# Kernel optimization log

Hardware: AMD Instinct MI355X
Metric: run time of the kernel (lower is better)

## Reference

```python
import jax, jax.numpy as jnp
import numpy as np

B, A, D, H = 32, 64, 128, 512
F = A * D  # 8192

def setup_inputs() -> dict:
    key = jax.random.key(0)
    ks = jax.random.split(key, 20)
    s = 0.02
    return {
        "swarm_states": jax.random.normal(ks[0], (B, A, D), jnp.float32),
        "swarm_goals": jax.random.normal(ks[1], (B, A, D), jnp.float32),
        # quantum layer stand-in: Linear(F->F) + tanh
        "Wq": jax.random.normal(ks[2], (F, F), jnp.float32) * s,
        "bq": jnp.zeros((F,), jnp.float32),
        # interaction_net: Linear(2D->H) ReLU Linear(H->H) ReLU Linear(H->D)
        "Wi1": jax.random.normal(ks[3], (2 * D, H), jnp.float32) * s,
        "bi1": jnp.zeros((H,), jnp.float32),
        "Wi2": jax.random.normal(ks[4], (H, H), jnp.float32) * s,
        "bi2": jnp.zeros((H,), jnp.float32),
        "Wi3": jax.random.normal(ks[5], (H, D), jnp.float32) * s,
        "bi3": jnp.zeros((D,), jnp.float32),
        # coordination_net: Linear(F->H) ReLU Linear(H->H) ReLU Linear(H->F)
        "Wc1": jax.random.normal(ks[6], (F, H), jnp.float32) * s,
        "bc1": jnp.zeros((H,), jnp.float32),
        "Wc2": jax.random.normal(ks[7], (H, H), jnp.float32) * s,
        "bc2": jnp.zeros((H,), jnp.float32),
        "Wc3": jax.random.normal(ks[8], (H, F), jnp.float32) * s,
        "bc3": jnp.zeros((F,), jnp.float32),
    }

def reference(swarm_states, swarm_goals, Wq, bq, Wi1, bi1, Wi2, bi2, Wi3, bi3,
              Wc1, bc1, Wc2, bc2, Wc3, bc3):
    b, a, d = swarm_states.shape
    states_flat = swarm_states.reshape(b, a * d)
    # quantum feature extraction (stand-in for QuantumNeuralLayer)
    quantum_features = jnp.tanh(states_flat @ Wq + bq)  # (B, A*D)

    # vectorized pairwise interaction MLP over all ordered (i, j) pairs
    xi = jnp.broadcast_to(swarm_states[:, :, None, :], (b, a, a, d))
    xj = jnp.broadcast_to(swarm_states[:, None, :, :], (b, a, a, d))
    pair = jnp.concatenate([xi, xj], axis=-1)            # (B, A, A, 2D)
    h = jax.nn.relu(pair @ Wi1 + bi1)
    h = jax.nn.relu(h @ Wi2 + bi2)
    inter = h @ Wi3 + bi3                                # (B, A, A, D)
    offdiag = (1.0 - jnp.eye(a, dtype=inter.dtype))[None, :, :, None]
    # per-agent aggregation over the other agents (mean over j != i)
    interactions = (inter * offdiag).sum(axis=2) / (a - 1)  # (B, A, D)

    c = jax.nn.relu(quantum_features @ Wc1 + bc1)
    c = jax.nn.relu(c @ Wc2 + bc2)
    coordination = (c @ Wc3 + bc3).reshape(b, a, d)      # (B, A, D)

    coordinated_states = swarm_states + 0.1 * interactions + 0.1 * coordination
    return coordinated_states, quantum_features, interactions, coordination
```

## Files before the change

### kernel.cpp

```cpp
#include <hip/hip_runtime.h>

typedef __attribute__((ext_vector_type(8))) short bf16x8;
typedef __attribute__((ext_vector_type(16))) float f32x16;
typedef _Float16 f16;
typedef __attribute__((ext_vector_type(8))) _Float16 f16x8;

static __device__ __forceinline__ unsigned short f2bf(float x) {
  unsigned int u = __float_as_uint(x);
  return (unsigned short)((u + 0x7FFFu + ((u >> 16) & 1u)) >> 16);
}
static __device__ __forceinline__ unsigned int pk2bf(float lo, float hi) {
  return ((unsigned int)f2bf(hi) << 16) | f2bf(lo);
}

static __device__ __forceinline__ f16x8 relu8(f16x8 x) {
  f16x8 z = {0, 0, 0, 0, 0, 0, 0, 0};
  return __builtin_elementwise_max(x, z);
}

__global__ __launch_bounds__(256) void tobf_kernel(const float* __restrict__ src,
                                                   unsigned short* __restrict__ dst) {
  const int idx = blockIdx.x * 256 + threadIdx.x;
  float4 v = ((const float4*)src)[idx];
  ushort4 o;
  o.x = f2bf(v.x); o.y = f2bf(v.y); o.z = f2bf(v.z); o.w = f2bf(v.w);
  ((ushort4*)dst)[idx] = o;
}

__global__ __launch_bounds__(256) void w2h_kernel(const float* __restrict__ Wi2,
                                                  f16* __restrict__ W2h) {
  __shared__ float tile[32][33];
  const int t = threadIdx.x;
  const int bk = blockIdx.x, bn = blockIdx.y;
  const int r = t >> 5, c = t & 31;
#pragma unroll
  for (int p = 0; p < 4; p++) {
    int rr = p * 8 + r;
    tile[rr][c] = Wi2[(bk * 32 + rr) * 512 + bn * 32 + c];
  }
  __syncthreads();
#pragma unroll
  for (int p = 0; p < 4; p++) {
    int rr = p * 8 + r;
    W2h[(bn * 32 + rr) * 512 + bk * 32 + c] = (f16)tile[c][rr];
  }
}

__global__ __launch_bounds__(256) void uvh_kernel(const float* __restrict__ S,
                                                  const float* __restrict__ Wi1,
                                                  const float* __restrict__ bi1,
                                                  f16* __restrict__ Uh, f16* __restrict__ Vh) {
  __shared__ float st[128][12];
  const int t = threadIdx.x;
  const int row0 = blockIdx.x * 8;
  for (int idx = t; idx < 1024; idx += 256) {
    int r = idx >> 7, k = idx & 127;
    st[k][r] = S[(row0 + r) * 128 + k];
  }
  __syncthreads();
  float au0[8], au1[8], av0[8], av1[8];
#pragma unroll
  for (int r = 0; r < 8; r++) { au0[r] = 0.f; au1[r] = 0.f; av0[r] = 0.f; av1[r] = 0.f; }
#pragma unroll 4
  for (int k = 0; k < 128; k++) {
    float wt0 = Wi1[k * 512 + t];
    float wt1 = Wi1[k * 512 + 256 + t];
    float wb0 = Wi1[(k + 128) * 512 + t];
    float wb1 = Wi1[(k + 128) * 512 + 256 + t];
    float4 sA = *(const float4*)&st[k][0];
    float4 sB = *(const float4*)&st[k][4];
    float s8[8] = {sA.x, sA.y, sA.z, sA.w, sB.x, sB.y, sB.z, sB.w};
#pragma unroll
    for (int r = 0; r < 8; r++) {
      au0[r] += s8[r] * wt0;
      au1[r] += s8[r] * wt1;
      av0[r] += s8[r] * wb0;
      av1[r] += s8[r] * wb1;
    }
  }
  const float b0 = bi1[t], b1 = bi1[256 + t];
#pragma unroll
  for (int r = 0; r < 8; r++) {
    Uh[(row0 + r) * 512 + t]       = (f16)(au0[r] + b0);
    Uh[(row0 + r) * 512 + 256 + t] = (f16)(au1[r] + b1);
    Vh[(row0 + r) * 512 + t]       = (f16)av0[r];
    Vh[(row0 + r) * 512 + 256 + t] = (f16)av1[r];
  }
}

__global__ __launch_bounds__(256, 4) void gemmw(const unsigned short* __restrict__ Abf,
                                                const float* __restrict__ W,
                                                float* __restrict__ P,
                                                int K, int N, int L, int l4sh) {
  __shared__ __align__(16) unsigned short As[32 * 512];
  const int t = threadIdx.x;
  const int k0 = blockIdx.y * L;
  const int L4 = L >> 2;
  const int swzm = 2 * L - 1;
  for (int idx = t; idx < (L << 3); idx += 256) {
    int row = idx >> l4sh, k4 = idx & (L4 - 1);
    ushort4 a4 = *(const ushort4*)&Abf[(size_t)row * K + k0 + k4 * 4];
    int off = (row * 2 * L + k4 * 8) ^ (((row & 7) << 4) & swzm);
    *(ushort4*)((char*)As + off) = a4;
  }
  __syncthreads();
  const int lane = t & 63, w = t >> 6;
  const int lrow = lane & 31, lh = lane >> 5;
  const int col = blockIdx.x * 128 + w * 32 + lrow;
  f32x16 acc0, acc1;
#pragma unroll
  for (int r = 0; r < 16; r++) { acc0[r] = 0.f; acc1[r] = 0.f; }
  const float* Wp = W + (size_t)(k0 + lh * 8) * N + col;
  const int aswz = ((lrow & 7) << 4) & swzm;
  const int abase = lrow * 2 * L + lh * 16;
  const int nks = L >> 4;
  int ks = 0;
  for (; ks + 1 < nks; ks += 2) {
    float wv0[8], wv1[8];
#pragma unroll
    for (int jj = 0; jj < 8; jj++) wv0[jj] = Wp[(size_t)(ks * 16 + jj) * N];
#pragma unroll
    for (int jj = 0; jj < 8; jj++) wv1[jj] = Wp[(size_t)(ks * 16 + 16 + jj) * N];
    uint4 b0, b1;
    b0.x = pk2bf(wv0[0], wv0[1]); b0.y = pk2bf(wv0[2], wv0[3]);
    b0.z = pk2bf(wv0[4], wv0[5]); b0.w = pk2bf(wv0[6], wv0[7]);
    b1.x = pk2bf(wv1[0], wv1[1]); b1.y = pk2bf(wv1[2], wv1[3]);
    b1.z = pk2bf(wv1[4], wv1[5]); b1.w = pk2bf(wv1[6], wv1[7]);
    bf16x8 af0 = *(const bf16x8*)((const char*)As + ((abase + ks * 32) ^ aswz));
    bf16x8 af1 = *(const bf16x8*)((const char*)As + ((abase + ks * 32 + 32) ^ aswz));
    acc0 = __builtin_amdgcn_mfma_f32_32x32x16_bf16(af0, *(const bf16x8*)&b0, acc0, 0, 0, 0);
    acc1 = __builtin_amdgcn_mfma_f32_32x32x16_bf16(af1, *(const bf16x8*)&b1, acc1, 0, 0, 0);
  }
  if (ks < nks) {
    float wv0[8];
#pragma unroll
    for (int jj = 0; jj < 8; jj++) wv0[jj] = Wp[(size_t)(ks * 16 + jj) * N];
    uint4 b0;
    b0.x = pk2bf(wv0[0], wv0[1]); b0.y = pk2bf(wv0[2], wv0[3]);
    b0.z = pk2bf(wv0[4], wv0[5]); b0.w = pk2bf(wv0[6], wv0[7]);
    bf16x8 af0 = *(const bf16x8*)((const char*)As + ((abase + ks * 32) ^ aswz));
    acc0 = __builtin_amdgcn_mfma_f32_32x32x16_bf16(af0, *(const bf16x8*)&b0, acc0, 0, 0, 0);
  }
  float* Pr = P + (size_t)blockIdx.y * 32 * N + col;
#pragma unroll
  for (int r = 0; r < 16; r++) {
    int row = (r & 3) + 8 * (r >> 2) + 4 * lh;
    Pr[(size_t)row * N] = acc0[r] + acc1[r];
  }
}

__global__ __launch_bounds__(256) void reduce_kernel(const float* __restrict__ P,
                                                     const float* __restrict__ bias,
                                                     float* __restrict__ dst,
                                                     unsigned short* __restrict__ dstbf,
                                                     int lnN, int KS, int act, int wbf) {
  const int idx = blockIdx.x * 256 + threadIdx.x;
  const int N = 1 << lnN;
  const int m = idx >> lnN, n = idx & (N - 1);
  float s = 0.f;
#pragma unroll 8
  for (int p = 0; p < KS; p++) s += P[((size_t)(p * 32 + m) << lnN) + n];
  s += bias[n];
  if (act == 1) s = fmaxf(s, 0.f);
  else if (act == 2) s = tanhf(s);
  dst[idx] = s;
  if (wbf) dstbf[idx] = f2bf(s);
}

__global__ __launch_bounds__(512, 2) void inter5_kernel(const f16* __restrict__ Uh,
                                                        const f16* __restrict__ Vh,
                                                        const f16* __restrict__ W2h,
                                                        const float* __restrict__ bi2,
                                                        float* __restrict__ Hsum) {
  __shared__ __align__(16) f16 Bt[128 * 512];
  const int t = threadIdx.x;
  const int nq = blockIdx.x;

#pragma unroll
  for (int i = 0; i < 16; i++) {
    int idx = i * 512 + t;
    int n = idx >> 6, ch = idx & 63;
    f16x8 w8 = *(const f16x8*)&W2h[(size_t)(nq * 128 + n) * 512 + ch * 8];
    int off = (n * 1024 + ch * 16) ^ ((n & 15) << 4);
    *(f16x8*)((char*)Bt + off) = w8;
  }
  __syncthreads();

  const int w = t >> 6, lane = t & 63;
  const int ii = w & 1, tg = w >> 1;
  const int lrow = lane & 31, lh = lane >> 5;
  const char* Btc = (const char*)Bt;

  int bofs[4], bswz[4];
#pragma unroll
  for (int nf = 0; nf < 4; nf++) {
    int nr = nf * 32 + lrow;
    bofs[nf] = nr * 1024 + lh * 16;
    bswz[nf] = (nr & 15) << 4;
  }

  for (int s = 0; s < 4; s++) {
    const int tid = blockIdx.y * 16 + tg * 4 + s;
    const int b = tid >> 5, it = tid & 31;
    const f16* Vb0 = Vh + (size_t)(b * 64 + lrow) * 512 + lh * 8;
    const f16* Vb1 = Vb0 + (size_t)32 * 512;
    const f16* Ub = Uh + (size_t)(b * 64 + it * 2 + ii) * 512 + lh * 8;

    f32x16 acc[2][4];
#pragma unroll
    for (int mf = 0; mf < 2; mf++)
#pragma unroll
      for (int nf = 0; nf < 4; nf++)
#pragma unroll
        for (int r = 0; r < 16; r++) acc[mf][nf][r] = 0.f;

    f16x8 v0 = *(const f16x8*)(Vb0);
    f16x8 v1 = *(const f16x8*)(Vb1);
    f16x8 u0 = *(const f16x8*)(Ub);
    f16x8 bf[4];
#pragma unroll
    for (int nf = 0; nf < 4; nf++) bf[nf] = *(const f16x8*)(Btc + (bofs[nf] ^ bswz[nf]));

#pragma unroll 2
    for (int kc = 0; kc < 512; kc += 16) {
      const int kn = (kc + 16) & 511;
      f16x8 v0n = *(const f16x8*)(Vb0 + kn);
      f16x8 v1n = *(const f16x8*)(Vb1 + kn);
      f16x8 u0n = *(const f16x8*)(Ub + kn);
      f16x8 bfn[4];
#pragma unroll
      for (int nf = 0; nf < 4; nf++)
        bfn[nf] = *(const f16x8*)(Btc + ((bofs[nf] + kn * 2) ^ bswz[nf]));
      f16x8 a0 = relu8(v0 + u0);
      f16x8 a1 = relu8(v1 + u0);
#pragma unroll
      for (int nf = 0; nf < 4; nf++) {
        acc[0][nf] = __builtin_amdgcn_mfma_f32_32x32x16_f16(a0, bf[nf], acc[0][nf], 0, 0, 0);
        acc[1][nf] = __builtin_amdgcn_mfma_f32_32x32x16_f16(a1, bf[nf], acc[1][nf], 0, 0, 0);
      }
      v0 = v0n; v1 = v1n; u0 = u0n;
#pragma unroll
      for (int nf = 0; nf < 4; nf++) bf[nf] = bfn[nf];
    }

    const int iglob = it * 2 + ii;
    const int mf_d = iglob >> 5;
    const int rd = iglob & 31;
    const int lh_d = (rd >> 2) & 1;
    const int r_d = (rd & 3) + 4 * (rd >> 3);
#pragma unroll
    for (int nf = 0; nf < 4; nf++) {
      const int col = nq * 128 + nf * 32 + lrow;
      const float b2 = bi2[col];
      float ssum = 0.f;
#pragma unroll
      for (int mf = 0; mf < 2; mf++)
#pragma unroll
        for (int r = 0; r < 16; r++) {
          float x = fmaxf(acc[mf][nf][r] + b2, 0.f);
          if (mf == mf_d && r == r_d && lh == lh_d) x = 0.f;
          ssum += x;
        }
      ssum += __shfl_xor(ssum, 32);
      if (lh == 0) Hsum[(size_t)(b * 64 + iglob) * 512 + col] = ssum;
    }
  }
}

__global__ __launch_bounds__(256) void k3_kernel(const float* __restrict__ Hsum,
                                                 const float* __restrict__ Wi3,
                                                 const float* __restrict__ bi3,
                                                 float* __restrict__ inter) {
  __shared__ float st[512][20];
  const int t = threadIdx.x;
  const int row0 = blockIdx.x * 16;
  for (int idx = t; idx < 8192; idx += 256) {
    int r = idx >> 9, k = idx & 511;
    st[k][r] = Hsum[(row0 + r) * 512 + k] * (1.0f / 63.0f);
  }
  __syncthreads();
  const int c = t & 63;
  const int rg = t >> 6;
  float a0[4] = {0.f, 0.f, 0.f, 0.f}, a1[4] = {0.f, 0.f, 0.f, 0.f};
#pragma unroll 4
  for (int k = 0; k < 512; k++) {
    float w0 = Wi3[k * 128 + c];
    float w1 = Wi3[k * 128 + 64 + c];
    float4 h = *(const float4*)&st[k][rg * 4];
    a0[0] += h.x * w0; a0[1] += h.y * w0; a0[2] += h.z * w0; a0[3] += h.w * w0;
    a1[0] += h.x * w1; a1[1] += h.y * w1; a1[2] += h.z * w1; a1[3] += h.w * w1;
  }
  float b0 = bi3[c], b1 = bi3[64 + c];
#pragma unroll
  for (int r = 0; r < 4; r++) {
    inter[(row0 + rg * 4 + r) * 128 + c]      = a0[r] + b0;
    inter[(row0 + rg * 4 + r) * 128 + 64 + c] = a1[r] + b1;
  }
}

__global__ __launch_bounds__(256) void combine_kernel(const float* __restrict__ S,
                                                      const float* __restrict__ inter,
                                                      const float* __restrict__ coord,
                                                      float* __restrict__ out0) {
  const int i = blockIdx.x * 256 + threadIdx.x;
  float4 s = ((const float4*)S)[i];
  float4 a = ((const float4*)inter)[i];
  float4 c = ((const float4*)coord)[i];
  float4 o;
  o.x = s.x + 0.1f * (a.x + c.x);
  o.y = s.y + 0.1f * (a.y + c.y);
  o.z = s.z + 0.1f * (a.z + c.z);
  o.w = s.w + 0.1f * (a.w + c.w);
  ((float4*)out0)[i] = o;
}

extern "C" void kernel_launch(void* const* d_in, const int* in_sizes, int n_in,
                              void* d_out, int out_size, void* d_ws, size_t ws_size,
                              hipStream_t stream) {
  const float* states = (const float*)d_in[0];
  const float* Wq  = (const float*)d_in[2];
  const float* bq  = (const float*)d_in[3];
  const float* Wi1 = (const float*)d_in[4];
  const float* bi1 = (const float*)d_in[5];
  const float* Wi2 = (const float*)d_in[6];
  const float* bi2 = (const float*)d_in[7];
  const float* Wi3 = (const float*)d_in[8];
  const float* bi3 = (const float*)d_in[9];
  const float* Wc1 = (const float*)d_in[10];
  const float* bc1 = (const float*)d_in[11];
  const float* Wc2 = (const float*)d_in[12];
  const float* bc2 = (const float*)d_in[13];
  const float* Wc3 = (const float*)d_in[14];
  const float* bc3 = (const float*)d_in[15];

  float* out   = (float*)d_out;
  float* out0  = out;
  float* qf    = out + 262144;
  float* inter = out + 524288;
  float* coord = out + 786432;

  char* ws = (char*)d_ws;
  float*          P    = (float*)(ws);
  f16*            Uh   = (f16*)(ws + ((size_t)16 << 20));
  f16*            Vh   = (f16*)(ws + ((size_t)19 << 20));
  f16*            W2h  = (f16*)(ws + ((size_t)22 << 20));
  float*          Hsum = (float*)(ws + ((size_t)23 << 20));
  unsigned short* Sbf  = (unsigned short*)(ws + ((size_t)27 << 20));
  unsigned short* qfbf = (unsigned short*)(ws + ((size_t)28 << 20));
  float*          c1   = (float*)(ws + ((size_t)29 << 20));
  float*          c2   = (float*)(ws + ((size_t)29 << 20) + (1 << 16));
  unsigned short* c1bf = (unsigned short*)(ws + ((size_t)29 << 20) + (2 << 16));
  unsigned short* c2bf = (unsigned short*)(ws + ((size_t)29 << 20) + (3 << 16));

  tobf_kernel<<<256, 256, 0, stream>>>(states, Sbf);
  w2h_kernel<<<dim3(16, 16), 256, 0, stream>>>(Wi2, W2h);
  uvh_kernel<<<256, 256, 0, stream>>>(states, Wi1, bi1, Uh, Vh);

  gemmw<<<dim3(64, 16), 256, 0, stream>>>(Sbf, Wq, P, 8192, 8192, 512, 7);
  reduce_kernel<<<1024, 256, 0, stream>>>(P, bq, qf, qfbf, 13, 16, 2, 1);

  inter5_kernel<<<dim3(4, 64), 512, 0, stream>>>(Uh, Vh, W2h, bi2, Hsum);
  k3_kernel<<<128, 256, 0, stream>>>(Hsum, Wi3, bi3, inter);

  gemmw<<<dim3(4, 64), 256, 0, stream>>>(qfbf, Wc1, P, 8192, 512, 128, 5);
  reduce_kernel<<<64, 256, 0, stream>>>(P, bc1, c1, c1bf, 9, 64, 1, 1);
  gemmw<<<dim3(4, 32), 256, 0, stream>>>(c1bf, Wc2, P, 512, 512, 16, 2);
  reduce_kernel<<<64, 256, 0, stream>>>(P, bc2, c2, c2bf, 9, 32, 1, 1);
  gemmw<<<dim3(64, 8), 256, 0, stream>>>(c2bf, Wc3, P, 512, 8192, 64, 4);
  reduce_kernel<<<1024, 256, 0, stream>>>(P, bc3, coord, qfbf, 13, 8, 0, 0);

  combine_kernel<<<256, 256, 0, stream>>>(states, inter, coord, out0);
}
```

Baseline: 240.6 us.

## Stage V tiles in shared memory for pairwise MLP and shrink k3 tiles

The pairwise interaction kernel now loads the V operand cooperatively into a swizzled 64x128 LDS chunk per K-block and reuses it across all waves. This replaces each wave's redundant global loads of V. Every block serves a single batch element, and the old register double-buffering of V and B loads is dropped. The k3 projection kernel handles 8 rows per block instead of 16, doubling the grid for more parallelism, at the cost of extra syncs per chunk and more LDS use.

```diff
diff --git a/kernel.cpp b/kernel.cpp
--- a/kernel.cpp
+++ b/kernel.cpp
@@ -167,12 +167,13 @@
   if (wbf) dstbf[idx] = f2bf(s);
 }
 
-__global__ __launch_bounds__(512, 2) void inter5_kernel(const f16* __restrict__ Uh,
+__global__ __launch_bounds__(512, 2) void inter6_kernel(const f16* __restrict__ Uh,
                                                         const f16* __restrict__ Vh,
                                                         const f16* __restrict__ W2h,
                                                         const float* __restrict__ bi2,
                                                         float* __restrict__ Hsum) {
   __shared__ __align__(16) f16 Bt[128 * 512];
+  __shared__ __align__(16) f16 Vc[64 * 128];
   const int t = threadIdx.x;
   const int nq = blockIdx.x;
 
@@ -184,12 +185,13 @@
     int off = (n * 1024 + ch * 16) ^ ((n & 15) << 4);
     *(f16x8*)((char*)Bt + off) = w8;
   }
-  __syncthreads();
 
   const int w = t >> 6, lane = t & 63;
   const int ii = w & 1, tg = w >> 1;
   const int lrow = lane & 31, lh = lane >> 5;
   const char* Btc = (const char*)Bt;
+  const char* Vcc = (const char*)Vc;
+  char* Vcw = (char*)Vc;
 
   int bofs[4], bswz[4];
 #pragma unroll
@@ -198,12 +200,16 @@
     bofs[nf] = nr * 1024 + lh * 16;
     bswz[nf] = (nr & 15) << 4;
   }
+  const int vofs0 = lrow * 256;
+  const int vswz0 = (lrow & 15) << 4;
+  const int vofs1 = (lrow + 32) * 256;
+  const int vswz1 = vswz0;
+
+  const int b = blockIdx.y >> 1;
 
   for (int s = 0; s < 4; s++) {
     const int tid = blockIdx.y * 16 + tg * 4 + s;
-    const int b = tid >> 5, it = tid & 31;
-    const f16* Vb0 = Vh + (size_t)(b * 64 + lrow) * 512 + lh * 8;
-    const f16* Vb1 = Vb0 + (size_t)32 * 512;
+    const int it = tid & 31;
     const f16* Ub = Uh + (size_t)(b * 64 + it * 2 + ii) * 512 + lh * 8;
 
     f32x16 acc[2][4];
@@ -214,33 +220,34 @@
 #pragma unroll
         for (int r = 0; r < 16; r++) acc[mf][nf][r] = 0.f;
 
-    f16x8 v0 = *(const f16x8*)(Vb0);
-    f16x8 v1 = *(const f16x8*)(Vb1);
-    f16x8 u0 = *(const f16x8*)(Ub);
-    f16x8 bf[4];
-#pragma unroll
-    for (int nf = 0; nf < 4; nf++) bf[nf] = *(const f16x8*)(Btc + (bofs[nf] ^ bswz[nf]));
-
-#pragma unroll 2
-    for (int kc = 0; kc < 512; kc += 16) {
-      const int kn = (kc + 16) & 511;
-      f16x8 v0n = *(const f16x8*)(Vb0 + kn);
-      f16x8 v1n = *(const f16x8*)(Vb1 + kn);
-      f16x8 u0n = *(const f16x8*)(Ub + kn);
-      f16x8 bfn[4];
-#pragma unroll
-      for (int nf = 0; nf < 4; nf++)
-        bfn[nf] = *(const f16x8*)(Btc + ((bofs[nf] + kn * 2) ^ bswz[nf]));
-      f16x8 a0 = relu8(v0 + u0);
-      f16x8 a1 = relu8(v1 + u0);
-#pragma unroll
-      for (int nf = 0; nf < 4; nf++) {
-        acc[0][nf] = __builtin_amdgcn_mfma_f32_32x32x16_f16(a0, bf[nf], acc[0][nf], 0, 0, 0);
-        acc[1][nf] = __builtin_amdgcn_mfma_f32_32x32x16_f16(a1, bf[nf], acc[1][nf], 0, 0, 0);
+    for (int ch = 0; ch < 4; ch++) {
+      const int kc = ch * 128;
+      __syncthreads();
+#pragma unroll
+      for (int i = 0; i < 2; i++) {
+        int idx = i * 512 + t;
+        int row = idx >> 4, c8 = idx & 15;
+        f16x8 w8 = *(const f16x8*)&Vh[(size_t)(b * 64 + row) * 512 + kc + c8 * 8];
+        *(f16x8*)(Vcw + ((row * 256 + c8 * 16) ^ ((row & 15) << 4))) = w8;
       }
-      v0 = v0n; v1 = v1n; u0 = u0n;
-#pragma unroll
-      for (int nf = 0; nf < 4; nf++) bf[nf] = bfn[nf];
+      __syncthreads();
+#pragma unroll
+      for (int k16 = 0; k16 < 8; k16++) {
+        const int kb2 = k16 * 32 + lh * 16;
+        f16x8 v0 = *(const f16x8*)(Vcc + ((vofs0 + kb2) ^ vswz0));
+        f16x8 v1 = *(const f16x8*)(Vcc + ((vofs1 + kb2) ^ vswz1));
+        f16x8 u0 = *(const f16x8*)(Ub + kc + k16 * 16);
+        f16x8 a0 = relu8(v0 + u0);
+        f16x8 a1 = relu8(v1 + u0);
+        const int kbyte = (kc + k16 * 16) * 2 + lh * 16 - lh * 16;
+        (void)kbyte;
+#pragma unroll
+        for (int nf = 0; nf < 4; nf++) {
+          f16x8 bfr = *(const f16x8*)(Btc + ((bofs[nf] + (kc + k16 * 16) * 2) ^ bswz[nf]));
+          acc[0][nf] = __builtin_amdgcn_mfma_f32_32x32x16_f16(a0, bfr, acc[0][nf], 0, 0, 0);
+          acc[1][nf] = __builtin_amdgcn_mfma_f32_32x32x16_f16(a1, bfr, acc[1][nf], 0, 0, 0);
+        }
+      }
     }
 
     const int iglob = it * 2 + ii;
@@ -271,30 +278,30 @@
                                                  const float* __restrict__ Wi3,
                                                  const float* __restrict__ bi3,
                                                  float* __restrict__ inter) {
-  __shared__ float st[512][20];
-  const int t = threadIdx.x;
-  const int row0 = blockIdx.x * 16;
-  for (int idx = t; idx < 8192; idx += 256) {
+  __shared__ float st[512][10];
+  const int t = threadIdx.x;
+  const int row0 = blockIdx.x * 8;
+  for (int idx = t; idx < 4096; idx += 256) {
     int r = idx >> 9, k = idx & 511;
     st[k][r] = Hsum[(row0 + r) * 512 + k] * (1.0f / 63.0f);
   }
   __syncthreads();
   const int c = t & 63;
   const int rg = t >> 6;
-  float a0[4] = {0.f, 0.f, 0.f, 0.f}, a1[4] = {0.f, 0.f, 0.f, 0.f};
+  float a0[2] = {0.f, 0.f}, a1[2] = {0.f, 0.f};
 #pragma unroll 4
   for (int k = 0; k < 512; k++) {
     float w0 = Wi3[k * 128 + c];
     float w1 = Wi3[k * 128 + 64 + c];
-    float4 h = *(const float4*)&st[k][rg * 4];
-    a0[0] += h.x * w0; a0[1] += h.y * w0; a0[2] += h.z * w0; a0[3] += h.w * w0;
-    a1[0] += h.x * w1; a1[1] += h.y * w1; a1[2] += h.z * w1; a1[3] += h.w * w1;
+    float2 h = *(const float2*)&st[k][rg * 2];
+    a0[0] += h.x * w0; a0[1] += h.y * w0;
+    a1[0] += h.x * w1; a1[1] += h.y * w1;
   }
   float b0 = bi3[c], b1 = bi3[64 + c];
 #pragma unroll
-  for (int r = 0; r < 4; r++) {
-    inter[(row0 + rg * 4 + r) * 128 + c]      = a0[r] + b0;
-    inter[(row0 + rg * 4 + r) * 128 + 64 + c] = a1[r] + b1;
+  for (int r = 0; r < 2; r++) {
+    inter[(row0 + rg * 2 + r) * 128 + c]      = a0[r] + b0;
+    inter[(row0 + rg * 2 + r) * 128 + 64 + c] = a1[r] + b1;
   }
 }
 
@@ -359,8 +366,8 @@
   gemmw<<<dim3(64, 16), 256, 0, stream>>>(Sbf, Wq, P, 8192, 8192, 512, 7);
   reduce_kernel<<<1024, 256, 0, stream>>>(P, bq, qf, qfbf, 13, 16, 2, 1);
 
-  inter5_kernel<<<dim3(4, 64), 512, 0, stream>>>(Uh, Vh, W2h, bi2, Hsum);
-  k3_kernel<<<128, 256, 0, stream>>>(Hsum, Wi3, bi3, inter);
+  inter6_kernel<<<dim3(4, 64), 512, 0, stream>>>(Uh, Vh, W2h, bi2, Hsum);
+  k3_kernel<<<256, 256, 0, stream>>>(Hsum, Wi3, bi3, inter);
 
   gemmw<<<dim3(4, 64), 256, 0, stream>>>(qfbf, Wc1, P, 8192, 512, 128, 5);
   reduce_kernel<<<64, 256, 0, stream>>>(P, bc1, c1, c1bf, 9, 64, 1, 1);
```

New measurement: 225.6 us. 6.2% less time.

## Reorder V to a k-blocked layout for coalesced MFMA loads, halve k3 rows per block

Applied to the files above, without the earlier changes.

The uvh kernel now writes V in a per-batch layout blocked by k-chunks of 8, so the 64 lanes of a wave load one contiguous 1 KB segment per k step in the pairwise MFMA kernel instead of striding across 1 KB rows. The interaction kernel's inner loop unroll is raised from 2 to 4. The k3 projection kernel processes 8 rows per block with 256 blocks instead of 16 rows with 128 blocks, for more parallelism. The scattered 2-byte stores in uvh may cost more, and the higher unroll raises register pressure.

```diff
diff --git a/kernel.cpp b/kernel.cpp
--- a/kernel.cpp
+++ b/kernel.cpp
@@ -49,7 +49,7 @@
 __global__ __launch_bounds__(256) void uvh_kernel(const float* __restrict__ S,
                                                   const float* __restrict__ Wi1,
                                                   const float* __restrict__ bi1,
-                                                  f16* __restrict__ Uh, f16* __restrict__ Vh) {
+                                                  f16* __restrict__ Uh, f16* __restrict__ Vg) {
   __shared__ float st[128][12];
   const int t = threadIdx.x;
   const int row0 = blockIdx.x * 8;
@@ -79,12 +79,15 @@
     }
   }
   const float b0 = bi1[t], b1 = bi1[256 + t];
+  const int kb = t >> 3, rem = t & 7;
 #pragma unroll
   for (int r = 0; r < 8; r++) {
-    Uh[(row0 + r) * 512 + t]       = (f16)(au0[r] + b0);
-    Uh[(row0 + r) * 512 + 256 + t] = (f16)(au1[r] + b1);
-    Vh[(row0 + r) * 512 + t]       = (f16)av0[r];
-    Vh[(row0 + r) * 512 + 256 + t] = (f16)av1[r];
+    const int row = row0 + r;
+    Uh[row * 512 + t]       = (f16)(au0[r] + b0);
+    Uh[row * 512 + 256 + t] = (f16)(au1[r] + b1);
+    const int j = row & 63, bb = row >> 6;
+    Vg[bb * 32768 + kb * 512 + j * 8 + rem]          = (f16)av0[r];
+    Vg[bb * 32768 + (kb + 32) * 512 + j * 8 + rem]   = (f16)av1[r];
   }
 }
 
@@ -167,8 +170,8 @@
   if (wbf) dstbf[idx] = f2bf(s);
 }
 
-__global__ __launch_bounds__(512, 2) void inter5_kernel(const f16* __restrict__ Uh,
-                                                        const f16* __restrict__ Vh,
+__global__ __launch_bounds__(512, 2) void inter7_kernel(const f16* __restrict__ Uh,
+                                                        const f16* __restrict__ Vg,
                                                         const f16* __restrict__ W2h,
                                                         const float* __restrict__ bi2,
                                                         float* __restrict__ Hsum) {
@@ -199,11 +202,12 @@
     bswz[nf] = (nr & 15) << 4;
   }
 
+  const int b = blockIdx.y >> 1;
+  const f16* Vbase = Vg + (size_t)b * 32768 + lh * 512 + lrow * 8;
+
   for (int s = 0; s < 4; s++) {
     const int tid = blockIdx.y * 16 + tg * 4 + s;
-    const int b = tid >> 5, it = tid & 31;
-    const f16* Vb0 = Vh + (size_t)(b * 64 + lrow) * 512 + lh * 8;
-    const f16* Vb1 = Vb0 + (size_t)32 * 512;
+    const int it = tid & 31;
     const f16* Ub = Uh + (size_t)(b * 64 + it * 2 + ii) * 512 + lh * 8;
 
     f32x16 acc[2][4];
@@ -214,18 +218,18 @@
 #pragma unroll
         for (int r = 0; r < 16; r++) acc[mf][nf][r] = 0.f;
 
-    f16x8 v0 = *(const f16x8*)(Vb0);
-    f16x8 v1 = *(const f16x8*)(Vb1);
+    f16x8 v0 = *(const f16x8*)(Vbase);
+    f16x8 v1 = *(const f16x8*)(Vbase + 256);
     f16x8 u0 = *(const f16x8*)(Ub);
     f16x8 bf[4];
 #pragma unroll
     for (int nf = 0; nf < 4; nf++) bf[nf] = *(const f16x8*)(Btc + (bofs[nf] ^ bswz[nf]));
 
-#pragma unroll 2
+#pragma unroll 4
     for (int kc = 0; kc < 512; kc += 16) {
       const int kn = (kc + 16) & 511;
-      f16x8 v0n = *(const f16x8*)(Vb0 + kn);
-      f16x8 v1n = *(const f16x8*)(Vb1 + kn);
+      f16x8 v0n = *(const f16x8*)(Vbase + kn * 64);
+      f16x8 v1n = *(const f16x8*)(Vbase + kn * 64 + 256);
       f16x8 u0n = *(const f16x8*)(Ub + kn);
       f16x8 bfn[4];
 #pragma unroll
@@ -271,30 +275,30 @@
                                                  const float* __restrict__ Wi3,
                                                  const float* __restrict__ bi3,
                                                  float* __restrict__ inter) {
-  __shared__ float st[512][20];
-  const int t = threadIdx.x;
-  const int row0 = blockIdx.x * 16;
-  for (int idx = t; idx < 8192; idx += 256) {
+  __shared__ float st[512][10];
+  const int t = threadIdx.x;
+  const int row0 = blockIdx.x * 8;
+  for (int idx = t; idx < 4096; idx += 256) {
     int r = idx >> 9, k = idx & 511;
     st[k][r] = Hsum[(row0 + r) * 512 + k] * (1.0f / 63.0f);
   }
   __syncthreads();
   const int c = t & 63;
   const int rg = t >> 6;
-  float a0[4] = {0.f, 0.f, 0.f, 0.f}, a1[4] = {0.f, 0.f, 0.f, 0.f};
+  float a0[2] = {0.f, 0.f}, a1[2] = {0.f, 0.f};
 #pragma unroll 4
   for (int k = 0; k < 512; k++) {
     float w0 = Wi3[k * 128 + c];
     float w1 = Wi3[k * 128 + 64 + c];
-    float4 h = *(const float4*)&st[k][rg * 4];
-    a0[0] += h.x * w0; a0[1] += h.y * w0; a0[2] += h.z * w0; a0[3] += h.w * w0;
-    a1[0] += h.x * w1; a1[1] += h.y * w1; a1[2] += h.z * w1; a1[3] += h.w * w1;
+    float2 h = *(const float2*)&st[k][rg * 2];
+    a0[0] += h.x * w0; a0[1] += h.y * w0;
+    a1[0] += h.x * w1; a1[1] += h.y * w1;
   }
   float b0 = bi3[c], b1 = bi3[64 + c];
 #pragma unroll
-  for (int r = 0; r < 4; r++) {
-    inter[(row0 + rg * 4 + r) * 128 + c]      = a0[r] + b0;
-    inter[(row0 + rg * 4 + r) * 128 + 64 + c] = a1[r] + b1;
+  for (int r = 0; r < 2; r++) {
+    inter[(row0 + rg * 2 + r) * 128 + c]      = a0[r] + b0;
+    inter[(row0 + rg * 2 + r) * 128 + 64 + c] = a1[r] + b1;
   }
 }
 
@@ -342,7 +346,7 @@
   char* ws = (char*)d_ws;
   float*          P    = (float*)(ws);
   f16*            Uh   = (f16*)(ws + ((size_t)16 << 20));
-  f16*            Vh   = (f16*)(ws + ((size_t)19 << 20));
+  f16*            Vg   = (f16*)(ws + ((size_t)19 << 20));
   f16*            W2h  = (f16*)(ws + ((size_t)22 << 20));
   float*          Hsum = (float*)(ws + ((size_t)23 << 20));
   unsigned short* Sbf  = (unsigned short*)(ws + ((size_t)27 << 20));
@@ -354,13 +358,13 @@
 
   tobf_kernel<<<256, 256, 0, stream>>>(states, Sbf);
   w2h_kernel<<<dim3(16, 16), 256, 0, stream>>>(Wi2, W2h);
-  uvh_kernel<<<256, 256, 0, stream>>>(states, Wi1, bi1, Uh, Vh);
+  uvh_kernel<<<256, 256, 0, stream>>>(states, Wi1, bi1, Uh, Vg);
 
   gemmw<<<dim3(64, 16), 256, 0, stream>>>(Sbf, Wq, P, 8192, 8192, 512, 7);
   reduce_kernel<<<1024, 256, 0, stream>>>(P, bq, qf, qfbf, 13, 16, 2, 1);
 
-  inter5_kernel<<<dim3(4, 64), 512, 0, stream>>>(Uh, Vh, W2h, bi2, Hsum);
-  k3_kernel<<<128, 256, 0, stream>>>(Hsum, Wi3, bi3, inter);
+  inter7_kernel<<<dim3(4, 64), 512, 0, stream>>>(Uh, Vg, W2h, bi2, Hsum);
+  k3_kernel<<<256, 256, 0, stream>>>(Hsum, Wi3, bi3, inter);
 
   gemmw<<<dim3(4, 64), 256, 0, stream>>>(qfbf, Wc1, P, 8192, 512, 128, 5);
   reduce_kernel<<<64, 256, 0, stream>>>(P, bc1, c1, c1bf, 9, 64, 1, 1);
```

New measurement: 233.3 us. -3.0%, faster.
